# Kernel tuning notes

Measured on AMD Instinct MI355X. Metric: run time of the kernel, lower is better.

Reference implementation:

```python
import jax, jax.numpy as jnp
import numpy as np

N_NODES = 50000
N_FEAT = 256
N_HID = 32
N_HEADS = 8
N_CLASSES = 32
N_EDGES = 800000
NEG_SLOPE = 0.2  # PyG GATConv default leaky_relu slope


def setup_inputs() -> dict:
    key = jax.random.key(0)
    ks = jax.random.split(key, 10)
    x = jax.random.normal(ks[0], (N_NODES, N_FEAT), dtype=jnp.float32)
    edge_index = jax.random.randint(ks[1], (2, N_EDGES), 0, N_NODES, dtype=jnp.int64)
    s1 = 1.0 / np.sqrt(N_FEAT)
    s2 = 1.0 / np.sqrt(N_HID * N_HEADS)
    W1 = jax.random.normal(ks[2], (N_FEAT, N_HEADS * N_HID), dtype=jnp.float32) * s1
    a_src1 = jax.random.normal(ks[3], (N_HEADS, N_HID), dtype=jnp.float32) * s1
    a_dst1 = jax.random.normal(ks[4], (N_HEADS, N_HID), dtype=jnp.float32) * s1
    b1 = jnp.zeros((N_HEADS * N_HID,), dtype=jnp.float32)
    W2 = jax.random.normal(ks[5], (N_HEADS * N_HID, N_CLASSES), dtype=jnp.float32) * s2
    a_src2 = jax.random.normal(ks[6], (1, N_CLASSES), dtype=jnp.float32) * s2
    a_dst2 = jax.random.normal(ks[7], (1, N_CLASSES), dtype=jnp.float32) * s2
    b2 = jnp.zeros((N_CLASSES,), dtype=jnp.float32)
    return {"x": x, "edge_index": edge_index, "W1": W1, "a_src1": a_src1,
            "a_dst1": a_dst1, "b1": b1, "W2": W2, "a_src2": a_src2,
            "a_dst2": a_dst2, "b2": b2}


def _gat_conv(h, src, dst, n_nodes, W, a_src, a_dst, heads, ch):
    # h: [N, F_in]; returns [N, heads, ch] aggregated per-node features
    z = (h @ W).reshape(n_nodes, heads, ch)           # [N,H,C]
    alpha_src = jnp.einsum('nhc,hc->nh', z, a_src)    # [N,H]
    alpha_dst = jnp.einsum('nhc,hc->nh', z, a_dst)    # [N,H]
    logits = jax.nn.leaky_relu(alpha_src[src] + alpha_dst[dst], NEG_SLOPE)  # [E,H]
    # segment softmax over incoming edges of each dst node
    m = jax.ops.segment_max(logits, dst, num_segments=n_nodes)  # [N,H]
    e = jnp.exp(logits - m[dst])                                 # [E,H]
    denom = jax.ops.segment_sum(e, dst, num_segments=n_nodes)   # [N,H]
    alpha = e / denom[dst]                                       # [E,H]
    msg = z[src] * alpha[:, :, None]                             # [E,H,C]
    return jax.ops.segment_sum(msg, dst, num_segments=n_nodes)  # [N,H,C]


def reference(x, edge_index, W1, a_src1, a_dst1, b1, W2, a_src2, a_dst2, b2):
    n = x.shape[0]
    # PyG GATConv default: add self loops
    loops = jnp.arange(n, dtype=edge_index.dtype)
    src = jnp.concatenate([edge_index[0], loops])
    dst = jnp.concatenate([edge_index[1], loops])
    h1 = _gat_conv(x, src, dst, n, W1, a_src1, a_dst1, N_HEADS, N_HID)
    h1 = h1.reshape(n, N_HEADS * N_HID) + b1          # concat=True
    h1 = jax.nn.elu(h1)
    # dropout is a no-op in eval mode
    h2 = _gat_conv(h1, src, dst, n, W2, a_src2, a_dst2, 1, N_CLASSES)
    out = h2.mean(axis=1) + b2                        # concat=False, heads=1
    return out
```

## Files before the change

### kernel.cpp

```cpp
#include <hip/hip_runtime.h>

#define NNODES 50000
#define NFEAT 256
#define NHID 32
#define NHEADS 8
#define NCLASSES 32
#define NEDGES 800000
#define ETOT (NEDGES + NNODES)
#define NSCAN_BLK 196
#define GEMM1_BLKS 782
#define SCAT_BLKS 3321
#define HIST_BLKS512 1661

typedef __attribute__((ext_vector_type(8))) short short8;
typedef __attribute__((ext_vector_type(4))) float f32x4;

__device__ __forceinline__ void get_edge(const int* __restrict__ ei, int e,
                                         int& s, int& d) {
    if (e < NEDGES) { s = ei[e]; d = ei[NEDGES + e]; }
    else            { s = e - NEDGES; d = s; }
}
__device__ __forceinline__ float lrelu(float x) { return x > 0.f ? x : 0.2f * x; }
__device__ __forceinline__ unsigned short f2bf(float f) {
    unsigned u = __float_as_uint(f);
    unsigned r = u + 0x7fffu + ((u >> 16) & 1u);
    return (unsigned short)(r >> 16);
}
__device__ __forceinline__ float bflo(unsigned u) { return __uint_as_float(u << 16); }
__device__ __forceinline__ float bfhi(unsigned u) { return __uint_as_float(u & 0xffff0000u); }

__global__ void wprep_k(const float* __restrict__ W1, const float* __restrict__ W2,
                        short8* __restrict__ W1frag, short8* __restrict__ W2frag) {
    int idx = blockIdx.x * 256 + threadIdx.x;
    if (idx < 8192) {
        int kc = idx >> 10, r = idx & 1023;
        int nt = r >> 6, lane = r & 63;
        int l16 = lane & 15, quad = lane >> 4;
        int n = nt * 16 + l16, k0 = kc * 32 + quad * 8;
        short8 v;
#pragma unroll
        for (int j = 0; j < 8; ++j) v[j] = (short)f2bf(W1[(k0 + j) * 256 + n]);
        W1frag[idx] = v;
    } else if (idx < 8192 + 1024) {
        int g = idx - 8192;
        int kc = g >> 7, r = g & 127;
        int nt = r >> 6, lane = r & 63;
        int l16 = lane & 15, quad = lane >> 4;
        int n = nt * 16 + l16, k0 = kc * 32 + quad * 8;
        short8 v;
#pragma unroll
        for (int j = 0; j < 8; ++j) v[j] = (short)f2bf(W2[(k0 + j) * 32 + n]);
        W2frag[g] = v;
    }
}

__global__ void scan_part_k(const int* __restrict__ deg, int* __restrict__ row_local,
                            int* __restrict__ bsum) {
    __shared__ int ws[4];
    int t = threadIdx.x, lane = t & 63, wid = t >> 6;
    int idx = blockIdx.x * 256 + t;
    int v = (idx < NNODES) ? deg[idx] : 0;
    int inc = v;
#pragma unroll
    for (int off = 1; off < 64; off <<= 1) {
        int u = __shfl_up(inc, off, 64);
        if (lane >= off) inc += u;
    }
    if (lane == 63) ws[wid] = inc;
    __syncthreads();
    int woff = 0;
#pragma unroll
    for (int j = 0; j < 4; ++j) woff += (j < wid) ? ws[j] : 0;
    if (idx < NNODES) row_local[idx] = woff + inc - v;
    if (t == 255) bsum[blockIdx.x] = woff + inc;
}

__global__ void scan_fix_k(const int* __restrict__ row_local, const int* __restrict__ bsum,
                           int* __restrict__ row_start) {
    __shared__ int ws[4];
    __shared__ int sboff;
    int t = threadIdx.x, lane = t & 63, wid = t >> 6;
    int v = (t < NSCAN_BLK) ? bsum[t] : 0;
    int inc = v;
#pragma unroll
    for (int off = 1; off < 64; off <<= 1) {
        int u = __shfl_up(inc, off, 64);
        if (lane >= off) inc += u;
    }
    if (lane == 63) ws[wid] = inc;
    __syncthreads();
    int woff = 0;
#pragma unroll
    for (int j = 0; j < 4; ++j) woff += (j < wid) ? ws[j] : 0;
    if (t == blockIdx.x) sboff = woff + inc - v;
    __syncthreads();
    int idx = blockIdx.x * 256 + t;
    if (idx < NNODES) row_start[idx] = row_local[idx] + sboff;
    if (idx == 0) row_start[NNODES] = ETOT;
}

__global__ __launch_bounds__(512) void gemm1_hist_k(
        const float* __restrict__ x, const short8* __restrict__ Wfrag,
        const float* __restrict__ av, const float* __restrict__ bv,
        unsigned short* __restrict__ z1, float* __restrict__ as_, float* __restrict__ ad_,
        const int* __restrict__ ei, int* __restrict__ deg,
        unsigned short* __restrict__ pos) {
    if (blockIdx.x >= GEMM1_BLKS) {
        int e = (blockIdx.x - GEMM1_BLKS) * 512 + threadIdx.x;
        if (e >= ETOT) return;
        int d = (e < NEDGES) ? ei[NEDGES + e] : (e - NEDGES);
        pos[e] = (unsigned short)atomicAdd(&deg[d], 1);
        return;
    }
    int t = threadIdx.x;
    int w = t >> 6, lane = t & 63;
    int rg = w >> 1, cb = w & 1;
    int quad = lane >> 4, l16 = lane & 15;
    int mA = blockIdx.x * 64 + rg * 16 + l16;
    int mAl = min(mA, NNODES - 1);

    const float4* xp = (const float4*)(x + (size_t)mAl * 256);
    short8 xreg[8];
#pragma unroll
    for (int kc = 0; kc < 8; ++kc) {
        float4 a0 = xp[kc * 8 + quad * 2];
        float4 a1 = xp[kc * 8 + quad * 2 + 1];
        short8 af;
        af[0] = (short)f2bf(a0.x); af[1] = (short)f2bf(a0.y);
        af[2] = (short)f2bf(a0.z); af[3] = (short)f2bf(a0.w);
        af[4] = (short)f2bf(a1.x); af[5] = (short)f2bf(a1.y);
        af[6] = (short)f2bf(a1.z); af[7] = (short)f2bf(a1.w);
        xreg[kc] = af;
    }

    f32x4 acc[8];
#pragma unroll
    for (int nt = 0; nt < 8; ++nt) acc[nt] = (f32x4){0.f, 0.f, 0.f, 0.f};

#pragma unroll
    for (int kc = 0; kc < 8; ++kc) {
        short8 af = xreg[kc];
#pragma unroll
        for (int nt = 0; nt < 8; ++nt) {
            short8 bf8 = Wfrag[kc * 1024 + (cb * 8 + nt) * 64 + lane];
            acc[nt] = __builtin_amdgcn_mfma_f32_16x16x32_bf16(af, bf8, acc[nt], 0, 0, 0);
        }
    }
    int mrow0 = blockIdx.x * 64 + rg * 16 + quad * 4;
#pragma unroll
    for (int nt = 0; nt < 8; ++nt) {
        int n = (cb * 8 + nt) * 16 + l16;
#pragma unroll
        for (int r = 0; r < 4; ++r) {
            int mr = mrow0 + r;
            if (mr < NNODES) z1[(size_t)mr * 256 + n] = f2bf(acc[nt][r]);
        }
    }
#pragma unroll
    for (int jj = 0; jj < 4; ++jj) {
        int h = cb * 4 + jj;
        float av0 = av[(cb * 8 + 2 * jj) * 16 + l16], av1v = av[(cb * 8 + 2 * jj + 1) * 16 + l16];
        float bv0 = bv[(cb * 8 + 2 * jj) * 16 + l16], bv1v = bv[(cb * 8 + 2 * jj + 1) * 16 + l16];
#pragma unroll
        for (int r = 0; r < 4; ++r) {
            float pa = acc[2 * jj][r] * av0 + acc[2 * jj + 1][r] * av1v;
            float pb = acc[2 * jj][r] * bv0 + acc[2 * jj + 1][r] * bv1v;
#pragma unroll
            for (int off = 1; off < 16; off <<= 1) {
                pa += __shfl_xor(pa, off, 64);
                pb += __shfl_xor(pb, off, 64);
            }
            int mr = mrow0 + r;
            if (l16 == 0 && mr < NNODES) { as_[mr * 8 + h] = pa; ad_[mr * 8 + h] = pb; }
        }
    }
}

__global__ void scatter_k(const int* __restrict__ ei, const int* __restrict__ row_start,
                          const unsigned short* __restrict__ pos, int* __restrict__ csr_src) {
    int e = blockIdx.x * 256 + threadIdx.x;
    if (e >= ETOT) return;
    int s, d;
    get_edge(ei, e, s, d);
    csr_src[row_start[d] + (int)pos[e]] = s;
}

__global__ __launch_bounds__(256) void gemm2_mfma_k(
        const unsigned short* __restrict__ h1, const short8* __restrict__ Wfrag,
        const float* __restrict__ av, const float* __restrict__ bv,
        unsigned short* __restrict__ z2b, float* __restrict__ as_, float* __restrict__ ad_) {
    int w = threadIdx.x >> 6, lane = threadIdx.x & 63;
    int quad = lane >> 4, l16 = lane & 15;
    int mA = blockIdx.x * 64 + w * 16 + l16;
    int mAl = min(mA, NNODES - 1);

    f32x4 acc[2];
    acc[0] = (f32x4){0.f, 0.f, 0.f, 0.f};
    acc[1] = (f32x4){0.f, 0.f, 0.f, 0.f};
    for (int kc = 0; kc < 8; ++kc) {
        int k0 = kc * 32 + quad * 8;
        short8 af = *(const short8*)(h1 + (size_t)mAl * 256 + k0);
#pragma unroll
        for (int nt = 0; nt < 2; ++nt) {
            short8 bf8 = Wfrag[kc * 128 + nt * 64 + lane];
            acc[nt] = __builtin_amdgcn_mfma_f32_16x16x32_bf16(af, bf8, acc[nt], 0, 0, 0);
        }
    }
    int mrow0 = blockIdx.x * 64 + w * 16 + quad * 4;
    float av0 = av[l16], av1v = av[16 + l16];
    float bv0 = bv[l16], bv1v = bv[16 + l16];
#pragma unroll
    for (int r = 0; r < 4; ++r) {
        int mr = mrow0 + r;
        float pa = acc[0][r] * av0 + acc[1][r] * av1v;
        float pb = acc[0][r] * bv0 + acc[1][r] * bv1v;
#pragma unroll
        for (int off = 1; off < 16; off <<= 1) {
            pa += __shfl_xor(pa, off, 64);
            pb += __shfl_xor(pb, off, 64);
        }
        if (mr < NNODES) {
            z2b[(size_t)mr * 32 + l16] = f2bf(acc[0][r]);
            z2b[(size_t)mr * 32 + 16 + l16] = f2bf(acc[1][r]);
            if (l16 == 0) { as_[mr] = pa; ad_[mr] = pb; }
        }
    }
}

__global__ void agg1_csr_k(const int* __restrict__ row_start, const int* __restrict__ csr_src,
                           const unsigned short* __restrict__ z, const float* __restrict__ as_,
                           const float* __restrict__ ad_, const float* __restrict__ b,
                           unsigned short* __restrict__ h1) {
    int wv = threadIdx.x >> 6, lane = threadIdx.x & 63;
    int d = blockIdx.x * 4 + wv;
    int h = lane >> 3;
    int c0 = lane * 4;
    int e8 = lane & 7;
    float adh = ad_[d * 8 + h];
    int beg = row_start[d], end = row_start[d + 1];
    float sum = 0.f, a0 = 0.f, a1 = 0.f, a2 = 0.f, a3 = 0.f;

    int idx = beg + e8;
    int sv = csr_src[idx < end ? idx : end - 1];
    float myw = __expf(lrelu(as_[sv * 8 + h] + adh));
    myw = (idx < end) ? myw : 0.f;

    for (int i = beg; i < end; i += 8) {
        int idx2 = i + 8 + e8;
        int sv2 = csr_src[idx2 < end ? idx2 : end - 1];
        float myw2 = __expf(lrelu(as_[sv2 * 8 + h] + adh));
        myw2 = (idx2 < end) ? myw2 : 0.f;

        int se[8];
        float we[8];
#pragma unroll
        for (int e = 0; e < 8; ++e) {
            se[e] = __shfl(sv, e, 64);
            we[e] = __shfl(myw, (lane & 56) | e, 64);
        }
        uint2 q[8];
#pragma unroll
        for (int e = 0; e < 8; ++e)
            q[e] = *(const uint2*)(z + (size_t)se[e] * 256 + c0);
#pragma unroll
        for (int e = 0; e < 8; ++e) {
            float wgt = we[e];
            sum += wgt;
            a0 += wgt * bflo(q[e].x);
            a1 += wgt * bfhi(q[e].x);
            a2 += wgt * bflo(q[e].y);
            a3 += wgt * bfhi(q[e].y);
        }
        sv = sv2;
        myw = myw2;
    }
    float inv = 1.f / sum;
    float o0 = a0 * inv + b[c0 + 0];
    float o1 = a1 * inv + b[c0 + 1];
    float o2 = a2 * inv + b[c0 + 2];
    float o3 = a3 * inv + b[c0 + 3];
    o0 = o0 > 0.f ? o0 : expm1f(o0);
    o1 = o1 > 0.f ? o1 : expm1f(o1);
    o2 = o2 > 0.f ? o2 : expm1f(o2);
    o3 = o3 > 0.f ? o3 : expm1f(o3);
    uint2 pk;
    pk.x = (unsigned)f2bf(o0) | ((unsigned)f2bf(o1) << 16);
    pk.y = (unsigned)f2bf(o2) | ((unsigned)f2bf(o3) << 16);
    *(uint2*)(h1 + (size_t)d * 256 + c0) = pk;
}

__global__ void agg2_csr_k(const int* __restrict__ row_start, const int* __restrict__ csr_src,
                           const unsigned short* __restrict__ z2b, const float* __restrict__ as_,
                           const float* __restrict__ ad_, const float* __restrict__ b,
                           float* __restrict__ out) {
    int g = blockIdx.x * 16 + (threadIdx.x >> 4);
    int l = threadIdx.x & 15;
    int lane = threadIdx.x & 63;
    int c0 = l * 2;
    int beg = row_start[g], end = row_start[g + 1];
    float adn = ad_[g];
    int e8 = l & 7;
    int gb = lane & 48;
    float sum = 0.f, a0 = 0.f, a1 = 0.f;

    int idx = beg + e8;
    int sv = csr_src[idx < end ? idx : end - 1];
    float myw = __expf(lrelu(as_[sv] + adn));
    myw = (idx < end) ? myw : 0.f;

    for (int i = beg; i < end; i += 8) {
        int idx2 = i + 8 + e8;
        int sv2 = csr_src[idx2 < end ? idx2 : end - 1];
        float myw2 = __expf(lrelu(as_[sv2] + adn));
        myw2 = (idx2 < end) ? myw2 : 0.f;

        int se[8];
        float we[8];
#pragma unroll
        for (int e = 0; e < 8; ++e) {
            se[e] = __shfl(sv, gb | e, 64);
            we[e] = __shfl(myw, gb | (8 | e), 64);
        }
        unsigned q[8];
#pragma unroll
        for (int e = 0; e < 8; ++e)
            q[e] = *(const unsigned*)(z2b + (size_t)se[e] * 32 + c0);
#pragma unroll
        for (int e = 0; e < 8; ++e) {
            float wgt = we[e];
            sum += wgt;
            a0 += wgt * bflo(q[e]);
            a1 += wgt * bfhi(q[e]);
        }
        sv = sv2;
        myw = myw2;
    }
    float inv = 1.f / sum;
    float2 o;
    o.x = a0 * inv + b[c0];
    o.y = a1 * inv + b[c0 + 1];
    *(float2*)(out + (size_t)g * 32 + c0) = o;
}

extern "C" void kernel_launch(void* const* d_in, const int* in_sizes, int n_in,
                              void* d_out, int out_size, void* d_ws, size_t ws_size,
                              hipStream_t stream) {
    const float* x   = (const float*)d_in[0];
    const int*   ei  = (const int*)d_in[1];
    const float* W1  = (const float*)d_in[2];
    const float* av1 = (const float*)d_in[3];
    const float* bv1 = (const float*)d_in[4];
    const float* b1  = (const float*)d_in[5];
    const float* W2  = (const float*)d_in[6];
    const float* av2 = (const float*)d_in[7];
    const float* bv2 = (const float*)d_in[8];
    const float* b2  = (const float*)d_in[9];
    float* out = (float*)d_out;

    unsigned short* z1 = (unsigned short*)d_ws;
    unsigned short* h1 = (unsigned short*)((float*)d_ws + 6400000);
    float* as1 = (float*)d_ws + 12800000;
    float* ad1 = as1 + 400000;
    unsigned short* z2b = (unsigned short*)(ad1 + 400000);
    float* as2 = ad1 + 400000 + 800000;
    float* ad2 = as2 + 50000;
    short8* W1frag = (short8*)(ad2 + 50000);
    short8* W2frag = W1frag + 8192;
    int* deg       = (int*)(ad2 + 50000) + 36864;
    int* row_start = deg + 50000;
    int* csr_src   = row_start + 50001;
    int* row_local = csr_src + 850000;
    int* bsum      = row_local + 50000;
    unsigned short* pos = (unsigned short*)z2b;

    hipMemsetAsync(deg, 0, (size_t)50000 * 4, stream);

    wprep_k<<<36, 256, 0, stream>>>(W1, W2, W1frag, W2frag);

    gemm1_hist_k<<<GEMM1_BLKS + HIST_BLKS512, 512, 0, stream>>>(
        x, W1frag, av1, bv1, z1, as1, ad1, ei, deg, pos);

    scan_part_k<<<NSCAN_BLK, 256, 0, stream>>>(deg, row_local, bsum);
    scan_fix_k<<<NSCAN_BLK, 256, 0, stream>>>(row_local, bsum, row_start);
    scatter_k<<<SCAT_BLKS, 256, 0, stream>>>(ei, row_start, pos, csr_src);

    agg1_csr_k<<<(NNODES + 3) / 4, 256, 0, stream>>>(row_start, csr_src, z1, as1, ad1, b1, h1);

    gemm2_mfma_k<<<(NNODES + 63) / 64, 256, 0, stream>>>(h1, W2frag, av2, bv2, z2b, as2, ad2);
    agg2_csr_k<<<NNODES / 16, 256, 0, stream>>>(row_start, csr_src, z2b, as2, ad2, b2, out);
}
```

Baseline: 272.5 us.

## Fuse scan and scatter into one cooperative kernel and fold memset into wprep

Replaces the two-pass degree scan and the edge scatter kernels with a single cooperative kernel that uses grid-wide syncs between the block scans, the block-offset fix-up, and the CSR scatter. The degree zeroing memset is moved into extra blocks of the weight-prep kernel. This removes two kernel launches and a memset from the stream. In exchange it pays for grid.sync barriers and relies on a 1024-block cooperative launch being co-resident on the device.

Measured after the change: 453.9 us. 66.6% more time.

```diff
diff --git a/kernel.cpp b/kernel.cpp
--- a/kernel.cpp
+++ b/kernel.cpp
@@ -1,4 +1,7 @@
 #include <hip/hip_runtime.h>
+#include <hip/hip_cooperative_groups.h>
+
+namespace cg = cooperative_groups;
 
 #define NNODES 50000
 #define NFEAT 256
@@ -9,8 +12,8 @@
 #define ETOT (NEDGES + NNODES)
 #define NSCAN_BLK 196
 #define GEMM1_BLKS 782
-#define SCAT_BLKS 3321
 #define HIST_BLKS512 1661
+#define CSRB_BLOCKS 1024
 
 typedef __attribute__((ext_vector_type(8))) short short8;
 typedef __attribute__((ext_vector_type(4))) float f32x4;
@@ -30,7 +33,13 @@
 __device__ __forceinline__ float bfhi(unsigned u) { return __uint_as_float(u & 0xffff0000u); }
 
 __global__ void wprep_k(const float* __restrict__ W1, const float* __restrict__ W2,
-                        short8* __restrict__ W1frag, short8* __restrict__ W2frag) {
+                        short8* __restrict__ W1frag, short8* __restrict__ W2frag,
+                        int* __restrict__ deg) {
+    if (blockIdx.x >= 36) {
+        int i = (blockIdx.x - 36) * 256 + threadIdx.x;
+        if (i < NNODES) deg[i] = 0;
+        return;
+    }
     int idx = blockIdx.x * 256 + threadIdx.x;
     if (idx < 8192) {
         int kc = idx >> 10, r = idx & 1023;
@@ -52,51 +61,6 @@
         for (int j = 0; j < 8; ++j) v[j] = (short)f2bf(W2[(k0 + j) * 32 + n]);
         W2frag[g] = v;
     }
-}
-
-__global__ void scan_part_k(const int* __restrict__ deg, int* __restrict__ row_local,
-                            int* __restrict__ bsum) {
-    __shared__ int ws[4];
-    int t = threadIdx.x, lane = t & 63, wid = t >> 6;
-    int idx = blockIdx.x * 256 + t;
-    int v = (idx < NNODES) ? deg[idx] : 0;
-    int inc = v;
-#pragma unroll
-    for (int off = 1; off < 64; off <<= 1) {
-        int u = __shfl_up(inc, off, 64);
-        if (lane >= off) inc += u;
-    }
-    if (lane == 63) ws[wid] = inc;
-    __syncthreads();
-    int woff = 0;
-#pragma unroll
-    for (int j = 0; j < 4; ++j) woff += (j < wid) ? ws[j] : 0;
-    if (idx < NNODES) row_local[idx] = woff + inc - v;
-    if (t == 255) bsum[blockIdx.x] = woff + inc;
-}
-
-__global__ void scan_fix_k(const int* __restrict__ row_local, const int* __restrict__ bsum,
-                           int* __restrict__ row_start) {
-    __shared__ int ws[4];
-    __shared__ int sboff;
-    int t = threadIdx.x, lane = t & 63, wid = t >> 6;
-    int v = (t < NSCAN_BLK) ? bsum[t] : 0;
-    int inc = v;
-#pragma unroll
-    for (int off = 1; off < 64; off <<= 1) {
-        int u = __shfl_up(inc, off, 64);
-        if (lane >= off) inc += u;
-    }
-    if (lane == 63) ws[wid] = inc;
-    __syncthreads();
-    int woff = 0;
-#pragma unroll
-    for (int j = 0; j < 4; ++j) woff += (j < wid) ? ws[j] : 0;
-    if (t == blockIdx.x) sboff = woff + inc - v;
-    __syncthreads();
-    int idx = blockIdx.x * 256 + t;
-    if (idx < NNODES) row_start[idx] = row_local[idx] + sboff;
-    if (idx == 0) row_start[NNODES] = ETOT;
 }
 
 __global__ __launch_bounds__(512) void gemm1_hist_k(
@@ -176,13 +140,63 @@
     }
 }
 
-__global__ void scatter_k(const int* __restrict__ ei, const int* __restrict__ row_start,
-                          const unsigned short* __restrict__ pos, int* __restrict__ csr_src) {
-    int e = blockIdx.x * 256 + threadIdx.x;
-    if (e >= ETOT) return;
-    int s, d;
-    get_edge(ei, e, s, d);
-    csr_src[row_start[d] + (int)pos[e]] = s;
+__global__ void csr_build_k(const int* __restrict__ deg, int* __restrict__ bsum,
+                            int* __restrict__ row_start, const int* __restrict__ ei,
+                            const unsigned short* __restrict__ pos,
+                            int* __restrict__ csr_src) {
+    cg::grid_group grid = cg::this_grid();
+    __shared__ int ws[4];
+    __shared__ int pre[256];
+    int t = threadIdx.x, lane = t & 63, wid = t >> 6;
+
+    for (int vb = blockIdx.x; vb < NSCAN_BLK; vb += gridDim.x) {
+        int idx = vb * 256 + t;
+        int v = (idx < NNODES) ? deg[idx] : 0;
+        int inc = v;
+#pragma unroll
+        for (int off = 1; off < 64; off <<= 1) {
+            int u = __shfl_up(inc, off, 64);
+            if (lane >= off) inc += u;
+        }
+        if (lane == 63) ws[wid] = inc;
+        __syncthreads();
+        int woff = 0;
+#pragma unroll
+        for (int j = 0; j < 4; ++j) woff += (j < wid) ? ws[j] : 0;
+        if (idx < NNODES) row_start[idx] = woff + inc - v;
+        if (t == 255) bsum[vb] = woff + inc;
+        __syncthreads();
+    }
+    grid.sync();
+
+    {
+        int v = (t < NSCAN_BLK) ? bsum[t] : 0;
+        int inc = v;
+#pragma unroll
+        for (int off = 1; off < 64; off <<= 1) {
+            int u = __shfl_up(inc, off, 64);
+            if (lane >= off) inc += u;
+        }
+        if (lane == 63) ws[wid] = inc;
+        __syncthreads();
+        int woff = 0;
+#pragma unroll
+        for (int j = 0; j < 4; ++j) woff += (j < wid) ? ws[j] : 0;
+        pre[t] = woff + inc - v;
+        __syncthreads();
+    }
+    for (int vb = blockIdx.x; vb < NSCAN_BLK; vb += gridDim.x) {
+        int idx = vb * 256 + t;
+        if (idx < NNODES) row_start[idx] += pre[vb];
+    }
+    if (blockIdx.x == 0 && t == 0) row_start[NNODES] = ETOT;
+    grid.sync();
+
+    for (int e = blockIdx.x * 256 + t; e < ETOT; e += gridDim.x * 256) {
+        int s, d;
+        get_edge(ei, e, s, d);
+        csr_src[row_start[d] + (int)pos[e]] = s;
+    }
 }
 
 __global__ __launch_bounds__(256) void gemm2_mfma_k(
@@ -373,16 +387,17 @@
     int* bsum      = row_local + 50000;
     unsigned short* pos = (unsigned short*)z2b;
 
-    hipMemsetAsync(deg, 0, (size_t)50000 * 4, stream);
-
-    wprep_k<<<36, 256, 0, stream>>>(W1, W2, W1frag, W2frag);
+    wprep_k<<<36 + NSCAN_BLK, 256, 0, stream>>>(W1, W2, W1frag, W2frag, deg);
 
     gemm1_hist_k<<<GEMM1_BLKS + HIST_BLKS512, 512, 0, stream>>>(
         x, W1frag, av1, bv1, z1, as1, ad1, ei, deg, pos);
 
-    scan_part_k<<<NSCAN_BLK, 256, 0, stream>>>(deg, row_local, bsum);
-    scan_fix_k<<<NSCAN_BLK, 256, 0, stream>>>(row_local, bsum, row_start);
-    scatter_k<<<SCAT_BLKS, 256, 0, stream>>>(ei, row_start, pos, csr_src);
+    {
+        void* cargs[] = {(void*)&deg, (void*)&bsum, (void*)&row_start,
+                         (void*)&ei, (void*)&pos, (void*)&csr_src};
+        hipLaunchCooperativeKernel((const void*)csr_build_k, dim3(CSRB_BLOCKS), dim3(256),
+                                   cargs, 0, stream);
+    }
 
     agg1_csr_k<<<(NNODES + 3) / 4, 256, 0, stream>>>(row_start, csr_src, z1, as1, ad1, b1, h1);
 
```

## Reorder CSR build: histogram with wprep, single-pass scan, scatter fused into GEMM1

Applied to the files above, without the earlier changes.

Moves the degree histogram into the weight-prep kernel and fuses the CSR scatter into the GEMM1 launch instead. The two scan kernels become one, with an agent-scope atomic counter acting as a grid barrier across its 196 blocks. This cuts the kernel count from six to three before aggregation and lets the scatter overlap the GEMM. The grid barrier assumes all scan blocks are co-resident, which holds for 196 blocks but is not guaranteed in general.

After: 293.6 us. 1.08x slower.

```diff
diff --git a/kernel.cpp b/kernel.cpp
--- a/kernel.cpp
+++ b/kernel.cpp
@@ -9,8 +9,8 @@
 #define ETOT (NEDGES + NNODES)
 #define NSCAN_BLK 196
 #define GEMM1_BLKS 782
-#define SCAT_BLKS 3321
-#define HIST_BLKS512 1661
+#define HIST_BLKS 3321
+#define SCAT_BLKS512 1661
 
 typedef __attribute__((ext_vector_type(8))) short short8;
 typedef __attribute__((ext_vector_type(4))) float f32x4;
@@ -29,34 +29,44 @@
 __device__ __forceinline__ float bflo(unsigned u) { return __uint_as_float(u << 16); }
 __device__ __forceinline__ float bfhi(unsigned u) { return __uint_as_float(u & 0xffff0000u); }
 
-__global__ void wprep_k(const float* __restrict__ W1, const float* __restrict__ W2,
-                        short8* __restrict__ W1frag, short8* __restrict__ W2frag) {
-    int idx = blockIdx.x * 256 + threadIdx.x;
-    if (idx < 8192) {
-        int kc = idx >> 10, r = idx & 1023;
-        int nt = r >> 6, lane = r & 63;
-        int l16 = lane & 15, quad = lane >> 4;
-        int n = nt * 16 + l16, k0 = kc * 32 + quad * 8;
-        short8 v;
-#pragma unroll
-        for (int j = 0; j < 8; ++j) v[j] = (short)f2bf(W1[(k0 + j) * 256 + n]);
-        W1frag[idx] = v;
-    } else if (idx < 8192 + 1024) {
-        int g = idx - 8192;
-        int kc = g >> 7, r = g & 127;
-        int nt = r >> 6, lane = r & 63;
-        int l16 = lane & 15, quad = lane >> 4;
-        int n = nt * 16 + l16, k0 = kc * 32 + quad * 8;
-        short8 v;
-#pragma unroll
-        for (int j = 0; j < 8; ++j) v[j] = (short)f2bf(W2[(k0 + j) * 32 + n]);
-        W2frag[g] = v;
-    }
-}
-
-__global__ void scan_part_k(const int* __restrict__ deg, int* __restrict__ row_local,
-                            int* __restrict__ bsum) {
+__global__ void wprep_hist_k(const float* __restrict__ W1, const float* __restrict__ W2,
+                             short8* __restrict__ W1frag, short8* __restrict__ W2frag,
+                             const int* __restrict__ ei, int* __restrict__ deg,
+                             unsigned short* __restrict__ pos) {
+    if (blockIdx.x < 36) {
+        int idx = blockIdx.x * 256 + threadIdx.x;
+        if (idx < 8192) {
+            int kc = idx >> 10, r = idx & 1023;
+            int nt = r >> 6, lane = r & 63;
+            int l16 = lane & 15, quad = lane >> 4;
+            int n = nt * 16 + l16, k0 = kc * 32 + quad * 8;
+            short8 v;
+#pragma unroll
+            for (int j = 0; j < 8; ++j) v[j] = (short)f2bf(W1[(k0 + j) * 256 + n]);
+            W1frag[idx] = v;
+        } else if (idx < 8192 + 1024) {
+            int g = idx - 8192;
+            int kc = g >> 7, r = g & 127;
+            int nt = r >> 6, lane = r & 63;
+            int l16 = lane & 15, quad = lane >> 4;
+            int n = nt * 16 + l16, k0 = kc * 32 + quad * 8;
+            short8 v;
+#pragma unroll
+            for (int j = 0; j < 8; ++j) v[j] = (short)f2bf(W2[(k0 + j) * 32 + n]);
+            W2frag[g] = v;
+        }
+    } else {
+        int e = (blockIdx.x - 36) * 256 + threadIdx.x;
+        if (e >= ETOT) return;
+        int d = (e < NEDGES) ? ei[NEDGES + e] : (e - NEDGES);
+        pos[e] = (unsigned short)atomicAdd(&deg[d], 1);
+    }
+}
+
+__global__ void csr_scan_k(const int* __restrict__ deg, int* __restrict__ bsum,
+                           int* __restrict__ row_start, int* __restrict__ ctr) {
     __shared__ int ws[4];
+    __shared__ int sboff;
     int t = threadIdx.x, lane = t & 63, wid = t >> 6;
     int idx = blockIdx.x * 256 + t;
     int v = (idx < NNODES) ? deg[idx] : 0;
@@ -71,45 +81,51 @@
     int woff = 0;
 #pragma unroll
     for (int j = 0; j < 4; ++j) woff += (j < wid) ? ws[j] : 0;
-    if (idx < NNODES) row_local[idx] = woff + inc - v;
-    if (t == 255) bsum[blockIdx.x] = woff + inc;
-}
-
-__global__ void scan_fix_k(const int* __restrict__ row_local, const int* __restrict__ bsum,
-                           int* __restrict__ row_start) {
-    __shared__ int ws[4];
-    __shared__ int sboff;
-    int t = threadIdx.x, lane = t & 63, wid = t >> 6;
-    int v = (t < NSCAN_BLK) ? bsum[t] : 0;
-    int inc = v;
-#pragma unroll
-    for (int off = 1; off < 64; off <<= 1) {
-        int u = __shfl_up(inc, off, 64);
-        if (lane >= off) inc += u;
-    }
-    if (lane == 63) ws[wid] = inc;
+    int local = woff + inc - v;
+    if (t == 255)
+        __hip_atomic_store(&bsum[blockIdx.x], woff + inc,
+                           __ATOMIC_RELEASE, __HIP_MEMORY_SCOPE_AGENT);
     __syncthreads();
-    int woff = 0;
-#pragma unroll
-    for (int j = 0; j < 4; ++j) woff += (j < wid) ? ws[j] : 0;
-    if (t == blockIdx.x) sboff = woff + inc - v;
+    if (t == 0) {
+        __hip_atomic_fetch_add(ctr, 1, __ATOMIC_ACQ_REL, __HIP_MEMORY_SCOPE_AGENT);
+        while (__hip_atomic_load(ctr, __ATOMIC_ACQUIRE, __HIP_MEMORY_SCOPE_AGENT) < NSCAN_BLK) {
+            __builtin_amdgcn_s_sleep(8);
+        }
+    }
     __syncthreads();
-    int idx = blockIdx.x * 256 + t;
-    if (idx < NNODES) row_start[idx] = row_local[idx] + sboff;
-    if (idx == 0) row_start[NNODES] = ETOT;
-}
-
-__global__ __launch_bounds__(512) void gemm1_hist_k(
+    {
+        int bv = (t < NSCAN_BLK) ? __hip_atomic_load(&bsum[t], __ATOMIC_ACQUIRE,
+                                                     __HIP_MEMORY_SCOPE_AGENT) : 0;
+        int binc = bv;
+#pragma unroll
+        for (int off = 1; off < 64; off <<= 1) {
+            int u = __shfl_up(binc, off, 64);
+            if (lane >= off) binc += u;
+        }
+        if (lane == 63) ws[wid] = binc;
+        __syncthreads();
+        int bwoff = 0;
+#pragma unroll
+        for (int j = 0; j < 4; ++j) bwoff += (j < wid) ? ws[j] : 0;
+        if (t == blockIdx.x) sboff = bwoff + binc - bv;
+        __syncthreads();
+    }
+    if (idx < NNODES) row_start[idx] = local + sboff;
+    if (blockIdx.x == 0 && t == 0) row_start[NNODES] = ETOT;
+}
+
+__global__ __launch_bounds__(512) void gemm1_scatter_k(
         const float* __restrict__ x, const short8* __restrict__ Wfrag,
         const float* __restrict__ av, const float* __restrict__ bv,
         unsigned short* __restrict__ z1, float* __restrict__ as_, float* __restrict__ ad_,
-        const int* __restrict__ ei, int* __restrict__ deg,
-        unsigned short* __restrict__ pos) {
+        const int* __restrict__ ei, const int* __restrict__ row_start,
+        const unsigned short* __restrict__ pos, int* __restrict__ csr_src) {
     if (blockIdx.x >= GEMM1_BLKS) {
         int e = (blockIdx.x - GEMM1_BLKS) * 512 + threadIdx.x;
         if (e >= ETOT) return;
-        int d = (e < NEDGES) ? ei[NEDGES + e] : (e - NEDGES);
-        pos[e] = (unsigned short)atomicAdd(&deg[d], 1);
+        int s, d;
+        get_edge(ei, e, s, d);
+        csr_src[row_start[d] + (int)pos[e]] = s;
         return;
     }
     int t = threadIdx.x;
@@ -174,15 +190,6 @@
             if (l16 == 0 && mr < NNODES) { as_[mr * 8 + h] = pa; ad_[mr * 8 + h] = pb; }
         }
     }
-}
-
-__global__ void scatter_k(const int* __restrict__ ei, const int* __restrict__ row_start,
-                          const unsigned short* __restrict__ pos, int* __restrict__ csr_src) {
-    int e = blockIdx.x * 256 + threadIdx.x;
-    if (e >= ETOT) return;
-    int s, d;
-    get_edge(ei, e, s, d);
-    csr_src[row_start[d] + (int)pos[e]] = s;
 }
 
 __global__ __launch_bounds__(256) void gemm2_mfma_k(
@@ -367,22 +374,20 @@
     short8* W1frag = (short8*)(ad2 + 50000);
     short8* W2frag = W1frag + 8192;
     int* deg       = (int*)(ad2 + 50000) + 36864;
-    int* row_start = deg + 50000;
+    int* ctr       = deg + 50000;
+    int* row_start = ctr + 4;
     int* csr_src   = row_start + 50001;
-    int* row_local = csr_src + 850000;
-    int* bsum      = row_local + 50000;
+    int* bsum      = csr_src + 850000;
     unsigned short* pos = (unsigned short*)z2b;
 
-    hipMemsetAsync(deg, 0, (size_t)50000 * 4, stream);
-
-    wprep_k<<<36, 256, 0, stream>>>(W1, W2, W1frag, W2frag);
-
-    gemm1_hist_k<<<GEMM1_BLKS + HIST_BLKS512, 512, 0, stream>>>(
-        x, W1frag, av1, bv1, z1, as1, ad1, ei, deg, pos);
-
-    scan_part_k<<<NSCAN_BLK, 256, 0, stream>>>(deg, row_local, bsum);
-    scan_fix_k<<<NSCAN_BLK, 256, 0, stream>>>(row_local, bsum, row_start);
-    scatter_k<<<SCAT_BLKS, 256, 0, stream>>>(ei, row_start, pos, csr_src);
+    hipMemsetAsync(deg, 0, (size_t)(50000 + 4) * 4, stream);
+
+    wprep_hist_k<<<36 + HIST_BLKS, 256, 0, stream>>>(W1, W2, W1frag, W2frag, ei, deg, pos);
+
+    csr_scan_k<<<NSCAN_BLK, 256, 0, stream>>>(deg, bsum, row_start, ctr);
+
+    gemm1_scatter_k<<<GEMM1_BLKS + SCAT_BLKS512, 512, 0, stream>>>(
+        x, W1frag, av1, bv1, z1, as1, ad1, ei, row_start, pos, csr_src);
 
     agg1_csr_k<<<(NNODES + 3) / 4, 256, 0, stream>>>(row_start, csr_src, z1, as1, ad1, b1, h1);
 
```
